# Kernel optimization log

Measured on AMD Instinct MI355X. Metric: run time of the kernel, lower is better.

## Reference

```python
import jax, jax.numpy as jnp
import numpy as np

B, C, F = 4096, 64, 128  # batch, num_channels (nodes), embedding_dim == hidden_dim
L = 3                    # num_layers


def setup_inputs() -> dict:
    key = jax.random.key(0)
    ks = jax.random.split(key, 2 * L + 3)
    s = 1.0 / np.sqrt(F)
    inp = {"embeddings": jax.random.normal(ks[0], (B, C, F), dtype=jnp.float32)}
    for l in range(L):
        inp[f"W{l}"] = jax.random.normal(ks[1 + 2 * l], (F, F), dtype=jnp.float32) * s
        inp[f"b{l}"] = jnp.zeros((F,), dtype=jnp.float32)
    inp["Wr"] = jax.random.normal(ks[2 * L + 1], (F, F), dtype=jnp.float32) * s
    inp["br"] = jnp.zeros((F,), dtype=jnp.float32)
    return inp


def reference(embeddings, W0, b0, W1, b1, W2, b2, Wr, br):
    # edge_index = all ordered pairs of distinct nodes (complete graph).
    # GCNConv adds self-loops and normalizes by D^{-1/2}(A+I)D^{-1/2};
    # on a complete graph every degree is C, so A_hat[i,j] = 1/C for all i,j.
    C_nodes = embeddings.shape[1]
    A_hat = jnp.full((C_nodes, C_nodes), 1.0 / C_nodes, dtype=embeddings.dtype)

    x = embeddings  # [B, C, F] — batch loop in the original is vectorized here
    for W, b in ((W0, b0), (W1, b1), (W2, b2)):
        xw = jnp.einsum("bcf,fh->bch", x, W)          # node-wise transform
        x = jax.nn.relu(jnp.einsum("cn,bnh->bch", A_hat, xw) + b)  # aggregate
    pooled = x.mean(axis=1)                            # [B, F] mean readout
    return pooled @ Wr + br                            # [B, F]
```

## Files before the change

### kernel.cpp

```cpp
#include <hip/hip_runtime.h>

#define B_ 4096
#define C_ 64
#define F_ 128
#define KP 136
#define GRP 32
#define NBLK (B_ / GRP)
#define WSLICE 8192
#define WLAYER 32768

typedef __attribute__((address_space(3))) unsigned int lds_u32;
typedef __attribute__((address_space(1))) unsigned int glb_u32;
typedef __attribute__((ext_vector_type(8))) short short8;
typedef __attribute__((ext_vector_type(4))) float f32x4;

__device__ __forceinline__ unsigned short bf16_trunc(float f) {
    union { float f; unsigned u; } v; v.f = f;
    return (unsigned short)(v.u >> 16);
}
__device__ __forceinline__ float bf16_tof(unsigned short h) {
    union { unsigned u; float f; } v; v.u = ((unsigned)h) << 16;
    return v.f;
}

__global__ __launch_bounds__(256) void mean_prep_kernel(const float* __restrict__ emb,
                                                        float* __restrict__ ebar,
                                                        const float* __restrict__ W0,
                                                        const float* __restrict__ W1,
                                                        const float* __restrict__ W2,
                                                        const float* __restrict__ Wr,
                                                        unsigned short* __restrict__ wprep) {
    __shared__ float4 part[8][32];
    __shared__ float  tile[128 * 17];

    const int b = blockIdx.x;
    const int t = threadIdx.x;
    const int fc = t & 31;
    const int cr = t >> 5;

    {
        const float4* src = (const float4*)(emb + (size_t)b * C_ * F_);
        float4 s = make_float4(0.f, 0.f, 0.f, 0.f);
        #pragma unroll
        for (int c = 0; c < C_ / 8; ++c) {
            float4 v = src[(cr + c * 8) * (F_ / 4) + fc];
            s.x += v.x; s.y += v.y; s.z += v.z; s.w += v.w;
        }
        part[cr][fc] = s;
        __syncthreads();
        if (t < 32) {
            float4 acc = part[0][t];
            #pragma unroll
            for (int i = 1; i < 8; ++i) {
                float4 v = part[i][t];
                acc.x += v.x; acc.y += v.y; acc.z += v.z; acc.w += v.w;
            }
            const float inv = 1.0f / (float)C_;
            acc.x *= inv; acc.y *= inv; acc.z *= inv; acc.w *= inv;
            ((float4*)(ebar + (size_t)b * F_))[t] = acc;
        }
    }

    if (b < 32) {
        const int layer = b >> 3;
        const int s     = b & 7;
        const float* W = layer == 0 ? W0 : layer == 1 ? W1 : layer == 2 ? W2 : Wr;

        {
            const int kk = t & 127, half = t >> 7;
            const float4* wr_ = (const float4*)(W + (size_t)kk * F_ + 16 * s + 8 * half);
            const float4 v0 = wr_[0], v1 = wr_[1];
            float* dst = tile + kk * 17 + 8 * half;
            dst[0] = v0.x; dst[1] = v0.y; dst[2] = v0.z; dst[3] = v0.w;
            dst[4] = v1.x; dst[5] = v1.y; dst[6] = v1.z; dst[7] = v1.w;
        }
        __syncthreads();
        {
            const int ln = t & 63;
            const int c = ln & 15, q = ln >> 4;
            const int kkpl_base = t >> 6;
            #pragma unroll
            for (int rep = 0; rep < 2; ++rep) {
                const int kkpl = kkpl_base + rep * 4;
                const int kk = kkpl >> 1, pl = kkpl & 1;
                unsigned wd[4];
                #pragma unroll
                for (int p = 0; p < 4; ++p) {
                    unsigned short u[2];
                    #pragma unroll
                    for (int h2 = 0; h2 < 2; ++h2) {
                        const int e = 2 * p + h2;
                        const float f = tile[(kk * 32 + q * 8 + e) * 17 + c];
                        const unsigned short hi = bf16_trunc(f);
                        u[h2] = (pl == 0) ? hi : bf16_trunc(f - bf16_tof(hi));
                    }
                    wd[p] = (unsigned)u[0] | ((unsigned)u[1] << 16);
                }
                const size_t dst = ((size_t)(layer * 4 + (s >> 1)) * 16
                                    + (size_t)((s & 1) * 8 + kkpl)) * 512 + ln * 8;
                *(int4*)(wprep + dst) = make_int4(wd[0], wd[1], wd[2], wd[3]);
            }
        }
    }
}

__device__ __forceinline__ void stage_w(const unsigned short* __restrict__ src,
                                        unsigned short* dst, int t) {
    #pragma unroll
    for (int i = 0; i < 16; ++i) {
        const int e = i * 2048 + t * 8;
        __builtin_amdgcn_global_load_lds((const glb_u32*)(src + e),
                                         (lds_u32*)(dst + e), 16, 0, 0);
    }
}

__global__ __launch_bounds__(256, 1) void mlp_mfma_kernel(
    const float* __restrict__ ebar,
    const unsigned short* __restrict__ wprep,
    const float* __restrict__ b0, const float* __restrict__ b1,
    const float* __restrict__ b2, const float* __restrict__ br,
    float* __restrict__ out)
{
    __shared__ unsigned short wb[2][WLAYER];
    __shared__ unsigned short x[2 * GRP * KP];

    const int t    = threadIdx.x;
    const int row0 = blockIdx.x * GRP;

    stage_w(wprep, wb[0], t);

    {
        const float4* src = (const float4*)(ebar + (size_t)row0 * F_);
        #pragma unroll
        for (int i = 0; i < 4; ++i) {
            const int idx = t + i * 256;
            const int r = idx >> 5, c4 = idx & 31;
            const float4 v = src[idx];
            ushort4 h, lo;
            h.x = bf16_trunc(v.x); lo.x = bf16_trunc(v.x - bf16_tof(h.x));
            h.y = bf16_trunc(v.y); lo.y = bf16_trunc(v.y - bf16_tof(h.y));
            h.z = bf16_trunc(v.z); lo.z = bf16_trunc(v.z - bf16_tof(h.z));
            h.w = bf16_trunc(v.w); lo.w = bf16_trunc(v.w - bf16_tof(h.w));
            *(ushort4*)&x[(0 * GRP + r) * KP + c4 * 4] = h;
            *(ushort4*)&x[(1 * GRP + r) * KP + c4 * 4] = lo;
        }
    }
    __syncthreads();

    const int w = t >> 6, l = t & 63;
    const int q = l >> 4, c = l & 15;

    const float* bs[4] = {b0, b1, b2, br};
    float biasr[4][2];
    #pragma unroll
    for (int L = 0; L < 4; ++L)
        #pragma unroll
        for (int i = 0; i < 2; ++i)
            biasr[L][i] = bs[L][(2 * w + i) * 16 + c];

    #pragma unroll
    for (int L = 0; L < 4; ++L) {
        if (L < 3) stage_w(wprep + (size_t)(L + 1) * WLAYER, wb[(L + 1) & 1], t);
        const unsigned short* ws = wb[L & 1] + w * WSLICE;

        f32x4 acc[2][2];
        #pragma unroll
        for (int rt = 0; rt < 2; ++rt)
            #pragma unroll
            for (int i = 0; i < 2; ++i)
                acc[rt][i] = (f32x4){0.f, 0.f, 0.f, 0.f};

        #pragma unroll
        for (int kk = 0; kk < 4; ++kk) {
            const int ko = kk * 32 + q * 8;
            const short8 ah0 = *(const short8*)&x[(0 * GRP + c)      * KP + ko];
            const short8 ah1 = *(const short8*)&x[(0 * GRP + 16 + c) * KP + ko];
            const short8 al0 = *(const short8*)&x[(1 * GRP + c)      * KP + ko];
            const short8 al1 = *(const short8*)&x[(1 * GRP + 16 + c) * KP + ko];
            #pragma unroll
            for (int i = 0; i < 2; ++i) {
                const short8 bh = *(const short8*)&ws[(i * 8 + kk * 2 + 0) * 512 + l * 8];
                const short8 bl = *(const short8*)&ws[(i * 8 + kk * 2 + 1) * 512 + l * 8];
                acc[0][i] = __builtin_amdgcn_mfma_f32_16x16x32_bf16(ah0, bh, acc[0][i], 0, 0, 0);
                acc[0][i] = __builtin_amdgcn_mfma_f32_16x16x32_bf16(al0, bh, acc[0][i], 0, 0, 0);
                acc[0][i] = __builtin_amdgcn_mfma_f32_16x16x32_bf16(ah0, bl, acc[0][i], 0, 0, 0);
                acc[1][i] = __builtin_amdgcn_mfma_f32_16x16x32_bf16(ah1, bh, acc[1][i], 0, 0, 0);
                acc[1][i] = __builtin_amdgcn_mfma_f32_16x16x32_bf16(al1, bh, acc[1][i], 0, 0, 0);
                acc[1][i] = __builtin_amdgcn_mfma_f32_16x16x32_bf16(ah1, bl, acc[1][i], 0, 0, 0);
            }
        }
        __syncthreads();

        if (L < 3) {
            #pragma unroll
            for (int rt = 0; rt < 2; ++rt)
                #pragma unroll
                for (int i = 0; i < 2; ++i)
                    #pragma unroll
                    for (int j = 0; j < 4; ++j) {
                        float v = acc[rt][i][j] + biasr[L][i];
                        v = fmaxf(v, 0.f);
                        const int row = rt * 16 + q * 4 + j;
                        const int col = (2 * w + i) * 16 + c;
                        const unsigned short h = bf16_trunc(v);
                        x[(0 * GRP + row) * KP + col] = h;
                        x[(1 * GRP + row) * KP + col] = bf16_trunc(v - bf16_tof(h));
                    }
            __syncthreads();
        } else {
            #pragma unroll
            for (int rt = 0; rt < 2; ++rt)
                #pragma unroll
                for (int i = 0; i < 2; ++i)
                    #pragma unroll
                    for (int j = 0; j < 4; ++j)
                        out[(size_t)(row0 + rt * 16 + q * 4 + j) * F_
                            + (2 * w + i) * 16 + c] = acc[rt][i][j] + biasr[3][i];
        }
    }
}

extern "C" void kernel_launch(void* const* d_in, const int* in_sizes, int n_in,
                              void* d_out, int out_size, void* d_ws, size_t ws_size,
                              hipStream_t stream) {
    const float* emb = (const float*)d_in[0];
    const float* W0  = (const float*)d_in[1];
    const float* b0  = (const float*)d_in[2];
    const float* W1  = (const float*)d_in[3];
    const float* b1  = (const float*)d_in[4];
    const float* W2  = (const float*)d_in[5];
    const float* b2  = (const float*)d_in[6];
    const float* Wr  = (const float*)d_in[7];
    const float* br  = (const float*)d_in[8];

    float*          ebar  = (float*)d_ws;
    unsigned short* wprep = (unsigned short*)((char*)d_ws + 2097152);

    mean_prep_kernel<<<B_, 256, 0, stream>>>(emb, ebar, W0, W1, W2, Wr, wprep);
    mlp_mfma_kernel<<<NBLK, 256, 0, stream>>>(ebar, wprep, b0, b1, b2, br,
                                              (float*)d_out);
}
```

Measured before the change: 33.62 us.

## Read MLP weights directly from global memory and halve rows per block

Removes the double-buffered LDS staging of each layer's prepared bf16 weights, so each wave now reads its weight fragments straight from global memory (L2-resident) inside the MFMA loop. The row group per block drops from 32 to 16, doubling the block count to 256, and launch bounds now allow two blocks per CU because LDS use shrinks to just the activation tile. This trades the weight-staging traffic and LDS footprint for more global loads on the MFMA critical path and no reuse of each weight fragment across two row tiles.

```diff
diff --git a/kernel.cpp b/kernel.cpp
--- a/kernel.cpp
+++ b/kernel.cpp
@@ -4,13 +4,11 @@
 #define C_ 64
 #define F_ 128
 #define KP 136
-#define GRP 32
+#define GRP 16
 #define NBLK (B_ / GRP)
 #define WSLICE 8192
 #define WLAYER 32768
 
-typedef __attribute__((address_space(3))) unsigned int lds_u32;
-typedef __attribute__((address_space(1))) unsigned int glb_u32;
 typedef __attribute__((ext_vector_type(8))) short short8;
 typedef __attribute__((ext_vector_type(4))) float f32x4;
 
@@ -104,35 +102,22 @@
     }
 }
 
-__device__ __forceinline__ void stage_w(const unsigned short* __restrict__ src,
-                                        unsigned short* dst, int t) {
-    #pragma unroll
-    for (int i = 0; i < 16; ++i) {
-        const int e = i * 2048 + t * 8;
-        __builtin_amdgcn_global_load_lds((const glb_u32*)(src + e),
-                                         (lds_u32*)(dst + e), 16, 0, 0);
-    }
-}
-
-__global__ __launch_bounds__(256, 1) void mlp_mfma_kernel(
+__global__ __launch_bounds__(256, 2) void mlp_mfma_kernel(
     const float* __restrict__ ebar,
     const unsigned short* __restrict__ wprep,
     const float* __restrict__ b0, const float* __restrict__ b1,
     const float* __restrict__ b2, const float* __restrict__ br,
     float* __restrict__ out)
 {
-    __shared__ unsigned short wb[2][WLAYER];
     __shared__ unsigned short x[2 * GRP * KP];
 
     const int t    = threadIdx.x;
     const int row0 = blockIdx.x * GRP;
 
-    stage_w(wprep, wb[0], t);
-
     {
         const float4* src = (const float4*)(ebar + (size_t)row0 * F_);
         #pragma unroll
-        for (int i = 0; i < 4; ++i) {
+        for (int i = 0; i < 2; ++i) {
             const int idx = t + i * 256;
             const int r = idx >> 5, c4 = idx & 31;
             const float4 v = src[idx];
@@ -160,62 +145,49 @@
 
     #pragma unroll
     for (int L = 0; L < 4; ++L) {
-        if (L < 3) stage_w(wprep + (size_t)(L + 1) * WLAYER, wb[(L + 1) & 1], t);
-        const unsigned short* ws = wb[L & 1] + w * WSLICE;
-
-        f32x4 acc[2][2];
-        #pragma unroll
-        for (int rt = 0; rt < 2; ++rt)
-            #pragma unroll
-            for (int i = 0; i < 2; ++i)
-                acc[rt][i] = (f32x4){0.f, 0.f, 0.f, 0.f};
+        const unsigned short* wl = wprep + (size_t)L * WLAYER + (size_t)w * WSLICE;
+
+        f32x4 acc[2];
+        acc[0] = (f32x4){0.f, 0.f, 0.f, 0.f};
+        acc[1] = (f32x4){0.f, 0.f, 0.f, 0.f};
 
         #pragma unroll
         for (int kk = 0; kk < 4; ++kk) {
             const int ko = kk * 32 + q * 8;
-            const short8 ah0 = *(const short8*)&x[(0 * GRP + c)      * KP + ko];
-            const short8 ah1 = *(const short8*)&x[(0 * GRP + 16 + c) * KP + ko];
-            const short8 al0 = *(const short8*)&x[(1 * GRP + c)      * KP + ko];
-            const short8 al1 = *(const short8*)&x[(1 * GRP + 16 + c) * KP + ko];
+            const short8 ah = *(const short8*)&x[(0 * GRP + c) * KP + ko];
+            const short8 al = *(const short8*)&x[(1 * GRP + c) * KP + ko];
             #pragma unroll
             for (int i = 0; i < 2; ++i) {
-                const short8 bh = *(const short8*)&ws[(i * 8 + kk * 2 + 0) * 512 + l * 8];
-                const short8 bl = *(const short8*)&ws[(i * 8 + kk * 2 + 1) * 512 + l * 8];
-                acc[0][i] = __builtin_amdgcn_mfma_f32_16x16x32_bf16(ah0, bh, acc[0][i], 0, 0, 0);
-                acc[0][i] = __builtin_amdgcn_mfma_f32_16x16x32_bf16(al0, bh, acc[0][i], 0, 0, 0);
-                acc[0][i] = __builtin_amdgcn_mfma_f32_16x16x32_bf16(ah0, bl, acc[0][i], 0, 0, 0);
-                acc[1][i] = __builtin_amdgcn_mfma_f32_16x16x32_bf16(ah1, bh, acc[1][i], 0, 0, 0);
-                acc[1][i] = __builtin_amdgcn_mfma_f32_16x16x32_bf16(al1, bh, acc[1][i], 0, 0, 0);
-                acc[1][i] = __builtin_amdgcn_mfma_f32_16x16x32_bf16(ah1, bl, acc[1][i], 0, 0, 0);
+                const short8 bh = *(const short8*)&wl[(size_t)(i * 8 + kk * 2 + 0) * 512 + l * 8];
+                const short8 bl = *(const short8*)&wl[(size_t)(i * 8 + kk * 2 + 1) * 512 + l * 8];
+                acc[i] = __builtin_amdgcn_mfma_f32_16x16x32_bf16(ah, bh, acc[i], 0, 0, 0);
+                acc[i] = __builtin_amdgcn_mfma_f32_16x16x32_bf16(al, bh, acc[i], 0, 0, 0);
+                acc[i] = __builtin_amdgcn_mfma_f32_16x16x32_bf16(ah, bl, acc[i], 0, 0, 0);
             }
         }
         __syncthreads();
 
         if (L < 3) {
             #pragma unroll
-            for (int rt = 0; rt < 2; ++rt)
+            for (int i = 0; i < 2; ++i)
                 #pragma unroll
-                for (int i = 0; i < 2; ++i)
-                    #pragma unroll
-                    for (int j = 0; j < 4; ++j) {
-                        float v = acc[rt][i][j] + biasr[L][i];
-                        v = fmaxf(v, 0.f);
-                        const int row = rt * 16 + q * 4 + j;
-                        const int col = (2 * w + i) * 16 + c;
-                        const unsigned short h = bf16_trunc(v);
-                        x[(0 * GRP + row) * KP + col] = h;
-                        x[(1 * GRP + row) * KP + col] = bf16_trunc(v - bf16_tof(h));
-                    }
+                for (int j = 0; j < 4; ++j) {
+                    float v = acc[i][j] + biasr[L][i];
+                    v = fmaxf(v, 0.f);
+                    const int row = q * 4 + j;
+                    const int col = (2 * w + i) * 16 + c;
+                    const unsigned short h = bf16_trunc(v);
+                    x[(0 * GRP + row) * KP + col] = h;
+                    x[(1 * GRP + row) * KP + col] = bf16_trunc(v - bf16_tof(h));
+                }
             __syncthreads();
         } else {
             #pragma unroll
-            for (int rt = 0; rt < 2; ++rt)
+            for (int i = 0; i < 2; ++i)
                 #pragma unroll
-                for (int i = 0; i < 2; ++i)
-                    #pragma unroll
-                    for (int j = 0; j < 4; ++j)
-                        out[(size_t)(row0 + rt * 16 + q * 4 + j) * F_
-                            + (2 * w + i) * 16 + c] = acc[rt][i][j] + biasr[3][i];
+                for (int j = 0; j < 4; ++j)
+                    out[(size_t)(row0 + q * 4 + j) * F_ + (2 * w + i) * 16 + c]
+                        = acc[i][j] + biasr[3][i];
         }
     }
 }
```

Measured after the change: 36.84 us. 1.1x slower.

## Load per-wave weight slices directly into registers with double-buffered prefetch

Applied to the files above, without the earlier changes.

Weight slices are no longer staged through a double-buffered LDS array with global_load_lds. Each wave now loads its own weight fragments straight from global memory into two register arrays and prefetches the next layer while computing the current one. This removes 128KB of LDS usage and the LDS read traffic for B operands, and it drops the barrier after the last layer. The cost is 32 short8 registers per lane, which risks register pressure or spills, plus direct global loads that depend on L2 hits.

```diff
diff --git a/kernel.cpp b/kernel.cpp
--- a/kernel.cpp
+++ b/kernel.cpp
@@ -9,8 +9,6 @@
 #define WSLICE 8192
 #define WLAYER 32768
 
-typedef __attribute__((address_space(3))) unsigned int lds_u32;
-typedef __attribute__((address_space(1))) unsigned int glb_u32;
 typedef __attribute__((ext_vector_type(8))) short short8;
 typedef __attribute__((ext_vector_type(4))) float f32x4;
 
@@ -104,16 +102,6 @@
     }
 }
 
-__device__ __forceinline__ void stage_w(const unsigned short* __restrict__ src,
-                                        unsigned short* dst, int t) {
-    #pragma unroll
-    for (int i = 0; i < 16; ++i) {
-        const int e = i * 2048 + t * 8;
-        __builtin_amdgcn_global_load_lds((const glb_u32*)(src + e),
-                                         (lds_u32*)(dst + e), 16, 0, 0);
-    }
-}
-
 __global__ __launch_bounds__(256, 1) void mlp_mfma_kernel(
     const float* __restrict__ ebar,
     const unsigned short* __restrict__ wprep,
@@ -121,13 +109,19 @@
     const float* __restrict__ b2, const float* __restrict__ br,
     float* __restrict__ out)
 {
-    __shared__ unsigned short wb[2][WLAYER];
     __shared__ unsigned short x[2 * GRP * KP];
 
     const int t    = threadIdx.x;
     const int row0 = blockIdx.x * GRP;
-
-    stage_w(wprep, wb[0], t);
+    const int w = t >> 6, l = t & 63;
+    const int q = l >> 4, c = l & 15;
+
+    const unsigned short* wbase = wprep + (size_t)w * WSLICE;
+
+    short8 wA[16], wB[16];
+    #pragma unroll
+    for (int f = 0; f < 16; ++f)
+        wA[f] = *(const short8*)&wbase[(size_t)f * 512 + l * 8];
 
     {
         const float4* src = (const float4*)(ebar + (size_t)row0 * F_);
@@ -147,9 +141,6 @@
     }
     __syncthreads();
 
-    const int w = t >> 6, l = t & 63;
-    const int q = l >> 4, c = l & 15;
-
     const float* bs[4] = {b0, b1, b2, br};
     float biasr[4][2];
     #pragma unroll
@@ -158,10 +149,13 @@
         for (int i = 0; i < 2; ++i)
             biasr[L][i] = bs[L][(2 * w + i) * 16 + c];
 
-    #pragma unroll
-    for (int L = 0; L < 4; ++L) {
-        if (L < 3) stage_w(wprep + (size_t)(L + 1) * WLAYER, wb[(L + 1) & 1], t);
-        const unsigned short* ws = wb[L & 1] + w * WSLICE;
+    auto layer_body = [&](int L, short8 (&CUR)[16], short8 (&NXT)[16]) {
+        if (L < 3) {
+            const unsigned short* nb = wbase + (size_t)(L + 1) * WLAYER;
+            #pragma unroll
+            for (int f = 0; f < 16; ++f)
+                NXT[f] = *(const short8*)&nb[(size_t)f * 512 + l * 8];
+        }
 
         f32x4 acc[2][2];
         #pragma unroll
@@ -179,8 +173,8 @@
             const short8 al1 = *(const short8*)&x[(1 * GRP + 16 + c) * KP + ko];
             #pragma unroll
             for (int i = 0; i < 2; ++i) {
-                const short8 bh = *(const short8*)&ws[(i * 8 + kk * 2 + 0) * 512 + l * 8];
-                const short8 bl = *(const short8*)&ws[(i * 8 + kk * 2 + 1) * 512 + l * 8];
+                const short8 bh = CUR[i * 8 + kk * 2 + 0];
+                const short8 bl = CUR[i * 8 + kk * 2 + 1];
                 acc[0][i] = __builtin_amdgcn_mfma_f32_16x16x32_bf16(ah0, bh, acc[0][i], 0, 0, 0);
                 acc[0][i] = __builtin_amdgcn_mfma_f32_16x16x32_bf16(al0, bh, acc[0][i], 0, 0, 0);
                 acc[0][i] = __builtin_amdgcn_mfma_f32_16x16x32_bf16(ah0, bl, acc[0][i], 0, 0, 0);
@@ -189,9 +183,9 @@
                 acc[1][i] = __builtin_amdgcn_mfma_f32_16x16x32_bf16(ah1, bl, acc[1][i], 0, 0, 0);
             }
         }
-        __syncthreads();
 
         if (L < 3) {
+            __syncthreads();
             #pragma unroll
             for (int rt = 0; rt < 2; ++rt)
                 #pragma unroll
@@ -217,7 +211,12 @@
                         out[(size_t)(row0 + rt * 16 + q * 4 + j) * F_
                             + (2 * w + i) * 16 + c] = acc[rt][i][j] + biasr[3][i];
         }
-    }
+    };
+
+    layer_body(0, wA, wB);
+    layer_body(1, wB, wA);
+    layer_body(2, wA, wB);
+    layer_body(3, wB, wA);
 }
 
 extern "C" void kernel_launch(void* const* d_in, const int* in_sizes, int n_in,
```

Result: faster. 31.25 us (-7.1%).
